# Kernel tuning notes

Measured on AMD Instinct MI355X. Metric: run time of the kernel, lower is better.

## Reference

```python
import jax, jax.numpy as jnp
import numpy as np

B, N, D, OUT = 8, 2048, 128, 128

def setup_inputs() -> dict:
    key = jax.random.key(0)
    k1, k2, k3, k4 = jax.random.split(key, 4)
    input_ = jax.random.normal(k1, (B, N, D), dtype=jnp.float32)
    adj_matrix = jax.random.randint(k2, (B, N, N), 0, 2, dtype=jnp.int32)
    W = jax.random.normal(k3, (2 * D, OUT), dtype=jnp.float32) * 0.05
    b = jax.random.normal(k4, (OUT,), dtype=jnp.float32) * 0.05
    return {"input_": input_, "adj_matrix": adj_matrix, "W": W, "b": b}

def reference(input_, adj_matrix, W, b):
    adj = adj_matrix.astype(jnp.float32)           # [B,N,N]
    deg = jnp.sum(adj, axis=2)                     # [B,N]
    deg = jnp.where(deg == 0, 1.0, deg)
    agg = jnp.einsum('bnm,bmd->bnd', adj, input_) / deg[:, :, None]  # mean aggregation
    feat = jnp.concatenate([input_, agg], axis=2)  # [B,N,2D]
    out = jax.nn.sigmoid(feat @ W + b)             # [B,N,OUT]
    out = out / jnp.linalg.norm(out, axis=2, keepdims=True)
    return out
```

## Files before the change

kernel.cpp:

```cpp
#include <hip/hip_runtime.h>

#define Bn 8
#define Nn 2048
#define Dn 128
#define OUTn 128

typedef __attribute__((ext_vector_type(8))) short bf16x8;
typedef __attribute__((ext_vector_type(8))) unsigned short ushort8;
typedef __attribute__((ext_vector_type(4))) float f32x4;
typedef __attribute__((ext_vector_type(4))) int int4v;
typedef __attribute__((ext_vector_type(4))) unsigned int uint4v;
typedef __attribute__((ext_vector_type(4))) float float4v;

__device__ __forceinline__ unsigned short f2bf(float f) {
  unsigned int u = __builtin_bit_cast(unsigned int, f);
  u += 0x7FFFu + ((u >> 16) & 1u);
  return (unsigned short)(u >> 16);
}

__global__ __launch_bounds__(256) void gcn_prep(const float* __restrict__ in,
                                                const float* __restrict__ W,
                                                unsigned short* __restrict__ inT,
                                                unsigned short* __restrict__ WT) {
  const int tid = threadIdx.x;
  if (blockIdx.x >= 256) {
    int gid = (blockIdx.x - 256) * 256 + tid;
    int j = gid >> 8, k = gid & 255;
    WT[gid] = f2bf(W[k * OUTn + j]);
    return;
  }
  const int b = blockIdx.x >> 5;
  const int n0 = (blockIdx.x & 31) * 64;
  __shared__ __attribute__((aligned(16))) unsigned short lds[64][130];
  #pragma unroll
  for (int c = 0; c < 32; ++c) {
    int e = tid + c * 256;
    int i = e >> 7, d = e & 127;
    lds[i][d] = f2bf(in[((size_t)(b * Nn + n0 + i)) * Dn + d]);
  }
  __syncthreads();
  #pragma unroll
  for (int c = 0; c < 4; ++c) {
    int ch = tid + c * 256;
    int d = ch >> 3, g = (ch & 7) * 8;
    ushort8 v;
    #pragma unroll
    for (int e = 0; e < 8; ++e) v[e] = lds[g + e][d];
    *(ushort8*)(inT + ((size_t)(b * Dn + d)) * Nn + n0 + g) = v;
  }
}

union SMem {
  struct {
    int A[2][32][64];
    unsigned short Bs[2][128][64];
  } s;
  struct {
    unsigned short aggl[32][136];
    float rowsum[32][2];
    float degs[32];
  } e;
};

#define STAGE(cur, kt)                                                         \
  {                                                                            \
    _Pragma("unroll")                                                          \
    for (int c = 0; c < 2; ++c) {                                              \
      const int r_ = c * 16 + wv * 4 + (l >> 4);                               \
      const int cg_ = (l & 15) ^ (r_ & 7);                                     \
      const int* gsrc_ = adjB + (size_t)r_ * Nn + (kt) * 64 + cg_ * 4;         \
      __builtin_amdgcn_global_load_lds(                                        \
          (const __attribute__((address_space(1))) void*)gsrc_,                \
          (__attribute__((address_space(3))) void*)((char*)&sm.s.A[cur][0][0] +\
                                                    c * 4096 + wv * 1024),     \
          16, 0, 0);                                                           \
    }                                                                          \
    _Pragma("unroll")                                                          \
    for (int c = 0; c < 4; ++c) {                                              \
      const int d_ = c * 32 + wv * 8 + (l >> 3);                               \
      const int cg_ = (l & 7) ^ (d_ & 7);                                      \
      const unsigned short* gsrc_ = inTb + (size_t)d_ * Nn + (kt) * 64 + cg_ * 8; \
      __builtin_amdgcn_global_load_lds(                                        \
          (const __attribute__((address_space(1))) void*)gsrc_,                \
          (__attribute__((address_space(3))) void*)((char*)&sm.s.Bs[cur][0][0] +\
                                                    c * 4096 + wv * 1024),     \
          16, 0, 0);                                                           \
    }                                                                          \
  }

#define COMPUTE(cur)                                                           \
  {                                                                            \
    _Pragma("unroll")                                                          \
    for (int kc = 0; kc < 2; ++kc) {                                           \
      const int c0_ = kc * 8 + lg * 2;                                         \
      int4v ai0 = *(const int4v*)(Abase + ((c0_ ^ swz8) * 16));                \
      int4v ai1 = *(const int4v*)(Abase + (((c0_ + 1) ^ swz8) * 16));          \
      dsum += ai0[0] + ai0[1] + ai0[2] + ai0[3] +                              \
              ai1[0] + ai1[1] + ai1[2] + ai1[3];                               \
      uint4v aw;                                                               \
      aw[0] = (unsigned)ai0[0] * 0x3F80u + (unsigned)ai0[1] * 0x3F800000u;     \
      aw[1] = (unsigned)ai0[2] * 0x3F80u + (unsigned)ai0[3] * 0x3F800000u;     \
      aw[2] = (unsigned)ai1[0] * 0x3F80u + (unsigned)ai1[1] * 0x3F800000u;     \
      aw[3] = (unsigned)ai1[2] * 0x3F80u + (unsigned)ai1[3] * 0x3F800000u;     \
      bf16x8 af = __builtin_bit_cast(bf16x8, aw);                              \
      _Pragma("unroll")                                                        \
      for (int cf = 0; cf < 4; ++cf) {                                         \
        bf16x8 bfm = *(const bf16x8*)(Bbase + (size_t)cf * 16 * 128 +          \
                                      (((kc * 4 + lg) ^ swz8) * 16));          \
        acc[cf] = __builtin_amdgcn_mfma_f32_16x16x32_bf16(af, bfm, acc[cf],    \
                                                          0, 0, 0);            \
      }                                                                        \
    }                                                                          \
  }

__global__ __launch_bounds__(256, 2) void gcn_main(
    const float* __restrict__ input_, const int* __restrict__ adj,
    const float* __restrict__ bvec, const unsigned short* __restrict__ inT,
    const unsigned short* __restrict__ WT, float* __restrict__ out) {
  __shared__ SMem sm;
  const int tid = threadIdx.x;
  const int wv = tid >> 6;
  const int l = tid & 63, lr = l & 15, lg = (l >> 4) & 3;
  const int rg = wv >> 1, ch = wv & 1;

  const int swz = (blockIdx.x & 7) * 64 + (blockIdx.x >> 3);
  const int bb = swz >> 6;
  const int row0 = (swz & 63) * 32;
  const int grow0 = bb * Nn + row0;

  const int* adjB = adj + (size_t)grow0 * Nn;
  const unsigned short* inTb = inT + (size_t)bb * Dn * Nn;

  const int swz8 = lr & 7;
  const char* Bbase0;
  f32x4 acc[4] = {};
  int dsum = 0;

  STAGE(0, 0);
  __syncthreads();

  #pragma unroll 1
  for (int ktp = 0; ktp < 16; ++ktp) {
    const int kt0 = 2 * ktp;
    {
      STAGE(1, kt0 + 1);
      const char* Abase = (const char*)&sm.s.A[0][0][0] + (rg * 16 + lr) * 256;
      const char* Bbase = (const char*)&sm.s.Bs[0][0][0] + (ch * 64 + lr) * 128;
      COMPUTE(0);
      __syncthreads();
    }
    {
      if (kt0 + 2 < 32) STAGE(0, kt0 + 2);
      const char* Abase = (const char*)&sm.s.A[1][0][0] + (rg * 16 + lr) * 256;
      const char* Bbase = (const char*)&sm.s.Bs[1][0][0] + (ch * 64 + lr) * 128;
      COMPUTE(1);
      __syncthreads();
    }
  }
  (void)Bbase0;

  {
    int s = dsum;
    s += __shfl_xor(s, 16);
    s += __shfl_xor(s, 32);
    if (l < 16) sm.e.degs[rg * 16 + l] = (s == 0) ? 1.0f : (float)s;
  }
  __syncthreads();

  float dgi[4];
  #pragma unroll
  for (int reg = 0; reg < 4; ++reg)
    dgi[reg] = 1.0f / sm.e.degs[rg * 16 + lg * 4 + reg];
  #pragma unroll
  for (int cf = 0; cf < 4; ++cf)
    #pragma unroll
    for (int reg = 0; reg < 4; ++reg)
      sm.e.aggl[rg * 16 + lg * 4 + reg][ch * 64 + cf * 16 + lr] =
          f2bf(acc[cf][reg] * dgi[reg]);
  __syncthreads();

  f32x4 acc2[4] = {};
  const float* xrow = input_ + (size_t)(grow0 + rg * 16 + lr) * Dn;
  #pragma unroll
  for (int ks = 0; ks < 8; ++ks) {
    bf16x8 af;
    if (ks < 4) {
      float4v f0 = *(const float4v*)(xrow + ks * 32 + lg * 8);
      float4v f1 = *(const float4v*)(xrow + ks * 32 + lg * 8 + 4);
      ushort8 vv;
      #pragma unroll
      for (int e = 0; e < 4; ++e) { vv[e] = f2bf(f0[e]); vv[e + 4] = f2bf(f1[e]); }
      af = __builtin_bit_cast(bf16x8, vv);
    } else {
      af = *(const bf16x8*)&sm.e.aggl[rg * 16 + lr][(ks - 4) * 32 + lg * 8];
    }
    #pragma unroll
    for (int cf = 0; cf < 4; ++cf) {
      bf16x8 bw = *(const bf16x8*)(WT + (size_t)(ch * 64 + cf * 16 + lr) * 256 +
                                   ks * 32 + lg * 8);
      acc2[cf] = __builtin_amdgcn_mfma_f32_16x16x32_bf16(af, bw, acc2[cf], 0, 0, 0);
    }
  }

  float bcol[4];
  #pragma unroll
  for (int cf = 0; cf < 4; ++cf) bcol[cf] = bvec[ch * 64 + cf * 16 + lr];
  float sg[4][4];
  #pragma unroll
  for (int cf = 0; cf < 4; ++cf)
    #pragma unroll
    for (int reg = 0; reg < 4; ++reg) {
      float x = acc2[cf][reg] + bcol[cf];
      sg[cf][reg] = 1.0f / (1.0f + expf(-x));
    }
  #pragma unroll
  for (int reg = 0; reg < 4; ++reg) {
    float p = 0.f;
    #pragma unroll
    for (int cf = 0; cf < 4; ++cf) p += sg[cf][reg] * sg[cf][reg];
    p += __shfl_xor(p, 1);
    p += __shfl_xor(p, 2);
    p += __shfl_xor(p, 4);
    p += __shfl_xor(p, 8);
    if (lr == 0) sm.e.rowsum[rg * 16 + lg * 4 + reg][ch] = p;
  }
  __syncthreads();
  #pragma unroll
  for (int reg = 0; reg < 4; ++reg) {
    const int row = rg * 16 + lg * 4 + reg;
    float nrm = rsqrtf(sm.e.rowsum[row][0] + sm.e.rowsum[row][1]);
    #pragma unroll
    for (int cf = 0; cf < 4; ++cf)
      out[(size_t)(grow0 + row) * OUTn + ch * 64 + cf * 16 + lr] =
          sg[cf][reg] * nrm;
  }
}

extern "C" void kernel_launch(void* const* d_in, const int* in_sizes, int n_in,
                              void* d_out, int out_size, void* d_ws, size_t ws_size,
                              hipStream_t stream) {
  (void)in_sizes; (void)n_in; (void)out_size; (void)ws_size;
  const float* input_ = (const float*)d_in[0];
  const int* adj = (const int*)d_in[1];
  const float* W = (const float*)d_in[2];
  const float* bvec = (const float*)d_in[3];
  float* out = (float*)d_out;

  unsigned short* inT = (unsigned short*)d_ws;
  unsigned short* WT = inT + (size_t)Bn * Dn * Nn;

  hipLaunchKernelGGL(gcn_prep, dim3(384), dim3(256), 0, stream, input_, W, inT, WT);
  hipLaunchKernelGGL(gcn_main, dim3(512), dim3(256), 0, stream,
                     input_, adj, bvec, inT, WT, out);
}
```

Before: 47.55 us.

## Triple-buffer adjacency/feature tiles with vmcnt-based waits and single barrier per step

```diff
diff --git a/kernel.cpp b/kernel.cpp
--- a/kernel.cpp
+++ b/kernel.cpp
@@ -52,8 +52,8 @@
 
 union SMem {
   struct {
-    int A[2][32][64];
-    unsigned short Bs[2][128][64];
+    int A[3][32][64];
+    unsigned short Bs[3][128][64];
   } s;
   struct {
     unsigned short aggl[32][136];
@@ -62,34 +62,35 @@
   } e;
 };
 
-#define STAGE(cur, kt)                                                         \
-  {                                                                            \
+#define STAGE(cur, kt) do {                                                    \
     _Pragma("unroll")                                                          \
-    for (int c = 0; c < 2; ++c) {                                              \
-      const int r_ = c * 16 + wv * 4 + (l >> 4);                               \
+    for (int c_ = 0; c_ < 2; ++c_) {                                           \
+      const int r_ = c_ * 16 + wv * 4 + (l >> 4);                              \
       const int cg_ = (l & 15) ^ (r_ & 7);                                     \
       const int* gsrc_ = adjB + (size_t)r_ * Nn + (kt) * 64 + cg_ * 4;         \
       __builtin_amdgcn_global_load_lds(                                        \
           (const __attribute__((address_space(1))) void*)gsrc_,                \
-          (__attribute__((address_space(3))) void*)((char*)&sm.s.A[cur][0][0] +\
-                                                    c * 4096 + wv * 1024),     \
+          (__attribute__((address_space(3))) void*)(smc + (cur) * 8192 +       \
+                                                   c_ * 4096 + wv * 1024),     \
           16, 0, 0);                                                           \
     }                                                                          \
     _Pragma("unroll")                                                          \
-    for (int c = 0; c < 4; ++c) {                                              \
-      const int d_ = c * 32 + wv * 8 + (l >> 3);                               \
+    for (int c_ = 0; c_ < 4; ++c_) {                                           \
+      const int d_ = c_ * 32 + wv * 8 + (l >> 3);                              \
       const int cg_ = (l & 7) ^ (d_ & 7);                                      \
       const unsigned short* gsrc_ = inTb + (size_t)d_ * Nn + (kt) * 64 + cg_ * 8; \
       __builtin_amdgcn_global_load_lds(                                        \
           (const __attribute__((address_space(1))) void*)gsrc_,                \
-          (__attribute__((address_space(3))) void*)((char*)&sm.s.Bs[cur][0][0] +\
-                                                    c * 4096 + wv * 1024),     \
+          (__attribute__((address_space(3))) void*)(smc + 24576 +              \
+                                                   (cur) * 16384 +             \
+                                                   c_ * 4096 + wv * 1024),     \
           16, 0, 0);                                                           \
     }                                                                          \
-  }
-
-#define COMPUTE(cur)                                                           \
-  {                                                                            \
+  } while (0)
+
+#define COMPUTE(cur) do {                                                      \
+    const char* Abase = smc + (cur) * 8192 + (rg * 16 + lr) * 256;             \
+    const char* Bbase = smc + 24576 + (cur) * 16384 + (ch * 64 + lr) * 128;    \
     _Pragma("unroll")                                                          \
     for (int kc = 0; kc < 2; ++kc) {                                           \
       const int c0_ = kc * 8 + lg * 2;                                         \
@@ -111,13 +112,20 @@
                                                           0, 0, 0);            \
       }                                                                        \
     }                                                                          \
-  }
+  } while (0)
+
+#define WAITBAR(N) do {                                                        \
+    asm volatile("s_waitcnt vmcnt(" #N ")" ::: "memory");                      \
+    __builtin_amdgcn_s_barrier();                                              \
+    __builtin_amdgcn_sched_barrier(0);                                         \
+  } while (0)
 
 __global__ __launch_bounds__(256, 2) void gcn_main(
     const float* __restrict__ input_, const int* __restrict__ adj,
     const float* __restrict__ bvec, const unsigned short* __restrict__ inT,
     const unsigned short* __restrict__ WT, float* __restrict__ out) {
   __shared__ SMem sm;
+  char* smc = (char*)&sm;
   const int tid = threadIdx.x;
   const int wv = tid >> 6;
   const int l = tid & 63, lr = l & 15, lg = (l >> 4) & 3;
@@ -132,32 +140,23 @@
   const unsigned short* inTb = inT + (size_t)bb * Dn * Nn;
 
   const int swz8 = lr & 7;
-  const char* Bbase0;
   f32x4 acc[4] = {};
   int dsum = 0;
 
   STAGE(0, 0);
-  __syncthreads();
+  STAGE(1, 1);
 
   #pragma unroll 1
-  for (int ktp = 0; ktp < 16; ++ktp) {
-    const int kt0 = 2 * ktp;
-    {
-      STAGE(1, kt0 + 1);
-      const char* Abase = (const char*)&sm.s.A[0][0][0] + (rg * 16 + lr) * 256;
-      const char* Bbase = (const char*)&sm.s.Bs[0][0][0] + (ch * 64 + lr) * 128;
-      COMPUTE(0);
-      __syncthreads();
-    }
-    {
-      if (kt0 + 2 < 32) STAGE(0, kt0 + 2);
-      const char* Abase = (const char*)&sm.s.A[1][0][0] + (rg * 16 + lr) * 256;
-      const char* Bbase = (const char*)&sm.s.Bs[1][0][0] + (ch * 64 + lr) * 128;
-      COMPUTE(1);
-      __syncthreads();
-    }
-  }
-  (void)Bbase0;
+  for (int j = 0; j < 10; ++j) {
+    const int kt = 3 * j;
+    WAITBAR(6); STAGE(2, kt + 2); COMPUTE(0);
+    WAITBAR(6); STAGE(0, kt + 3); COMPUTE(1);
+    WAITBAR(6); STAGE(1, kt + 4); COMPUTE(2);
+  }
+  WAITBAR(6); COMPUTE(0);
+  WAITBAR(0); COMPUTE(1);
+
+  __syncthreads();
 
   {
     int s = dsum;
```

Measured after the change: 43.67 us. 8.1% less time.
